# Optimization experiments

Hardware: AMD Instinct MI355X
Metric: run time of the kernel (lower is better)

The kernel has to match this reference:

```python
import jax, jax.numpy as jnp
import numpy as np

V = 32000   # vocab_size
T = 2048    # train_len (pos embed table size)
E = 1024    # embed_dim
H = 16      # num_heads
FF = 4096   # ff_dim
L = 4       # num_layers
B, C = 2, 1024
D = E // H  # head_dim = 64
EPS = 1e-5


def setup_inputs() -> dict:
    key = jax.random.key(0)
    ks = jax.random.split(key, 12)
    s = 0.02
    inp = {
        "x": jax.random.randint(ks[0], (B, C), 0, V),
        "embed": jax.random.normal(ks[1], (V, E), jnp.float32) * s,
        "pos_embed": jax.random.normal(ks[2], (T, E), jnp.float32) * s,
        "Wq": jax.random.normal(ks[3], (L, E, E), jnp.float32) * s,
        "Wk": jax.random.normal(ks[4], (L, E, E), jnp.float32) * s,
        "Wv": jax.random.normal(ks[5], (L, E, E), jnp.float32) * s,
        "Wo": jax.random.normal(ks[6], (L, E, E), jnp.float32) * s,
        "ln1_w": jnp.ones((L, E), jnp.float32),
        "ln1_b": jnp.zeros((L, E), jnp.float32),
        "ln2_w": jnp.ones((L, E), jnp.float32),
        "ln2_b": jnp.zeros((L, E), jnp.float32),
        "W1": jax.random.normal(ks[7], (L, E, FF), jnp.float32) * s,
        "b1": jnp.zeros((L, FF), jnp.float32),
        "W2": jax.random.normal(ks[8], (L, FF, E), jnp.float32) * s,
        "b2": jnp.zeros((L, E), jnp.float32),
        "lnf_w": jnp.ones((E,), jnp.float32),
        "lnf_b": jnp.zeros((E,), jnp.float32),
        "Wout": jax.random.normal(ks[9], (E, V), jnp.float32) * s,
        "bout": jnp.zeros((V,), jnp.float32),
    }
    return inp


def _layernorm(h, w, b):
    mu = jnp.mean(h, axis=-1, keepdims=True)
    var = jnp.var(h, axis=-1, keepdims=True)
    return (h - mu) * jax.lax.rsqrt(var + EPS) * w + b


def reference(x, embed, pos_embed, Wq, Wk, Wv, Wo, ln1_w, ln1_b, ln2_w, ln2_b,
              W1, b1, W2, b2, lnf_w, lnf_b, Wout, bout):
    Bx, Cx = x.shape
    positions = jnp.clip(jnp.arange(Cx), 0, T - 1)  # 'clamp' extrapolation
    h = embed[x] + pos_embed[positions]             # [B,C,E]
    # causal mask: -inf above the diagonal
    mask = jnp.where(jnp.tril(jnp.ones((Cx, Cx), bool)), 0.0, -jnp.inf).astype(h.dtype)
    scale = 1.0 / np.sqrt(D)
    for i in range(L):
        hn = _layernorm(h, ln1_w[i], ln1_b[i])
        Q = (hn @ Wq[i]).reshape(Bx, Cx, H, D).transpose(0, 2, 1, 3)  # [B,H,C,D]
        K = (hn @ Wk[i]).reshape(Bx, Cx, H, D).transpose(0, 2, 1, 3)
        Vv = (hn @ Wv[i]).reshape(Bx, Cx, H, D).transpose(0, 2, 1, 3)
        scores = jnp.einsum('bhqd,bhkd->bhqk', Q, K) * scale + mask
        weights = jax.nn.softmax(scores, axis=-1)
        attn = jnp.einsum('bhqk,bhkd->bhqd', weights, Vv)
        attn = attn.transpose(0, 2, 1, 3).reshape(Bx, Cx, E) @ Wo[i]
        h = h + attn
        hn2 = _layernorm(h, ln2_w[i], ln2_b[i])
        h = h + jax.nn.gelu(hn2 @ W1[i] + b1[i], approximate=False) @ W2[i] + b2[i]
    return _layernorm(h, lnf_w, lnf_b) @ Wout + bout  # [B,C,V]
```

## Files before the change

### kernel.cpp

```cpp
#include <hip/hip_runtime.h>
#include <hip/hip_bf16.h>
#include <math.h>

constexpr int V  = 32000;
constexpr int E  = 1024;
constexpr int H  = 16;
constexpr int FF = 4096;
constexpr int L  = 4;
constexpr int B  = 2;
constexpr int C  = 1024;
constexpr int D  = 64;
constexpr int N  = B * C;
constexpr int E3 = 3 * E;
constexpr float EPS = 1e-5f;

typedef __hip_bfloat16 bf16;
typedef __bf16 bf16x8 __attribute__((ext_vector_type(8)));
typedef __bf16 bf16x4 __attribute__((ext_vector_type(4)));
typedef float  f32x4  __attribute__((ext_vector_type(4)));

#define AS1 __attribute__((address_space(1)))
#define AS3 __attribute__((address_space(3)))

__device__ inline bf16x8 lds_load8(const bf16* p) {
    bf16x4 lo = *(const bf16x4*)p;
    bf16x4 hi = *(const bf16x4*)(p + 4);
    bf16x8 r;
    r[0]=lo[0]; r[1]=lo[1]; r[2]=lo[2]; r[3]=lo[3];
    r[4]=hi[0]; r[5]=hi[1]; r[6]=hi[2]; r[7]=hi[3];
    return r;
}
__device__ inline void lds_store8(bf16* p, bf16x8 v) {
    bf16x4 lo, hi;
    lo[0]=v[0]; lo[1]=v[1]; lo[2]=v[2]; lo[3]=v[3];
    hi[0]=v[4]; hi[1]=v[5]; hi[2]=v[6]; hi[3]=v[7];
    *(bf16x4*)p = lo; *(bf16x4*)(p + 4) = hi;
}

__device__ inline bf16x8 lds_frag(const bf16* sbase, int row, int chunk) {
    return *(const bf16x8*)(sbase + (row >> 3) * 512 + (row & 7) * 64 +
                            ((chunk ^ (row & 7)) << 3));
}

__global__ void embed_kernel(const int* __restrict__ x,
                             const float* __restrict__ embed,
                             const float* __restrict__ pos,
                             float* __restrict__ h) {
    int token = blockIdx.x;
    int c = token % C;
    int id = x[token];
    const float* erow = embed + (size_t)id * E;
    const float* prow = pos   + (size_t)c  * E;
    float* hrow = h + (size_t)token * E;
    for (int e = threadIdx.x; e < E; e += blockDim.x)
        hrow[e] = erow[e] + prow[e];
}

__global__ void layernorm_kernel(const float* __restrict__ in,
                                 const float* __restrict__ w,
                                 const float* __restrict__ b,
                                 bf16* __restrict__ out) {
    __shared__ float red[256];
    int token = blockIdx.x;
    int tid = threadIdx.x;
    float4 xv = ((const float4*)(in + (size_t)token * E))[tid];

    red[tid] = xv.x + xv.y + xv.z + xv.w;
    __syncthreads();
    for (int st = 128; st > 0; st >>= 1) {
        if (tid < st) red[tid] += red[tid + st];
        __syncthreads();
    }
    float mu = red[0] * (1.0f / E);
    __syncthreads();

    float d0 = xv.x - mu, d1 = xv.y - mu, d2 = xv.z - mu, d3 = xv.w - mu;
    red[tid] = d0 * d0 + d1 * d1 + d2 * d2 + d3 * d3;
    __syncthreads();
    for (int st = 128; st > 0; st >>= 1) {
        if (tid < st) red[tid] += red[tid + st];
        __syncthreads();
    }
    float var = red[0] * (1.0f / E);
    float inv = rsqrtf(var + EPS);

    float4 wv = ((const float4*)w)[tid];
    float4 bv = ((const float4*)b)[tid];
    float y0 = d0 * inv * wv.x + bv.x;
    float y1 = d1 * inv * wv.y + bv.y;
    float y2 = d2 * inv * wv.z + bv.z;
    float y3 = d3 * inv * wv.w + bv.w;
    ushort4 o;
    { bf16 t0 = __float2bfloat16(y0); o.x = *(ushort*)&t0; }
    { bf16 t1 = __float2bfloat16(y1); o.y = *(ushort*)&t1; }
    { bf16 t2 = __float2bfloat16(y2); o.z = *(ushort*)&t2; }
    { bf16 t3 = __float2bfloat16(y3); o.w = *(ushort*)&t3; }
    ((ushort4*)(out + (size_t)token * E))[tid] = o;
}

__global__ void transpose_bf16(const float* __restrict__ in,
                               bf16* __restrict__ out, int K, int Nn) {
    __shared__ float tile[32][33];
    int n0 = blockIdx.x * 32, k0 = blockIdx.y * 32;
    int tx = threadIdx.x & 31, ty = threadIdx.x >> 5;
    #pragma unroll
    for (int i = 0; i < 32; i += 8)
        tile[ty + i][tx] = in[(size_t)(k0 + ty + i) * Nn + n0 + tx];
    __syncthreads();
    #pragma unroll
    for (int i = 0; i < 32; i += 8)
        out[(size_t)(n0 + ty + i) * K + k0 + tx] = __float2bfloat16(tile[tx][ty + i]);
}

__global__ void transpose_v(const bf16* __restrict__ qkv,
                            bf16* __restrict__ vt) {
    __shared__ ushort tile[32][34];
    int c0 = blockIdx.x * 32;
    int d0 = (blockIdx.y & 1) * 32;
    int bh = blockIdx.y >> 1;
    int bb = bh >> 4, hh = bh & 15;
    int tx = threadIdx.x & 31, ty = threadIdx.x >> 5;
    const ushort* src = (const ushort*)qkv;
    ushort* dst = (ushort*)vt;
    #pragma unroll
    for (int i = 0; i < 32; i += 8)
        tile[ty + i][tx] = src[(size_t)(bb * C + c0 + ty + i) * E3 + 2 * E + hh * D + d0 + tx];
    __syncthreads();
    #pragma unroll
    for (int i = 0; i < 32; i += 8)
        dst[((size_t)bh * D + d0 + ty + i) * C + c0 + tx] = tile[tx][ty + i];
}

__launch_bounds__(256, 2)
__global__ void gemm_bf16_128(const bf16* __restrict__ A,
                              const bf16* __restrict__ Bt,
                              const float* __restrict__ bias,
                              const float* __restrict__ res,
                              float* __restrict__ outF,
                              bf16*  __restrict__ outB,
                              int M, int Nc, int K, int gelu_flag) {
    __shared__ __align__(16) bf16 sA[2][128 * 64];
    __shared__ __align__(16) bf16 sB[2][128 * 64];

    int tid  = threadIdx.x;
    int lane = tid & 63;
    int wid  = tid >> 6;
    int wr   = wid >> 1;
    int wc   = wid & 1;
    int l16  = lane & 15;
    int lhi  = lane >> 4;

    int nwg = gridDim.x * gridDim.y;
    int id  = blockIdx.y * gridDim.x + blockIdx.x;
    int cpx = nwg >> 3;
    int swz = (id & 7) * cpx + (id >> 3);
    int bx  = swz / gridDim.y;
    int by  = swz % gridDim.y;

    size_t brow = (size_t)by * 128;
    size_t bcol = (size_t)bx * 128;

    f32x4 acc[4][4] = {};

    auto stage = [&](int buf, int t) {
        size_t k0 = (size_t)t * 64;
        #pragma unroll
        for (int s = 0; s < 4; ++s) {
            int slot = s * 256 + tid;
            int row  = slot >> 3;
            int ch   = (slot & 7) ^ (row & 7);
            int ldso = (s * 256 + wid * 64) * 8;
            const bf16* ga = A + (brow + row) * K + k0 + ch * 8;
            __builtin_amdgcn_global_load_lds(
                (const AS1 void*)ga, (AS3 void*)(&sA[buf][0] + ldso), 16, 0, 0);
        }
        #pragma unroll
        for (int s = 0; s < 4; ++s) {
            int slot = s * 256 + tid;
            int row  = slot >> 3;
            int ch   = (slot & 7) ^ (row & 7);
            int ldso = (s * 256 + wid * 64) * 8;
            const bf16* gb = Bt + (bcol + row) * K + k0 + ch * 8;
            __builtin_amdgcn_global_load_lds(
                (const AS1 void*)gb, (AS3 void*)(&sB[buf][0] + ldso), 16, 0, 0);
        }
    };

    int NT = K / 64;
    stage(0, 0);

    for (int t = 0; t < NT; ++t) {
        if (t + 1 < NT) {
            stage((t + 1) & 1, t + 1);
            asm volatile("s_waitcnt vmcnt(8)" ::: "memory");
        } else {
            asm volatile("s_waitcnt vmcnt(0)" ::: "memory");
        }
        __builtin_amdgcn_sched_barrier(0);
        __builtin_amdgcn_s_barrier();

        const bf16* As_ = &sA[t & 1][0];
        const bf16* Bs_ = &sB[t & 1][0];
        bf16x8 ra[4][2], rb[4][2];
        #pragma unroll
        for (int m = 0; m < 4; ++m)
            #pragma unroll
            for (int kh = 0; kh < 2; ++kh)
                ra[m][kh] = lds_frag(As_, wr * 64 + m * 16 + l16, kh * 4 + lhi);
        #pragma unroll
        for (int n = 0; n < 4; ++n)
            #pragma unroll
            for (int kh = 0; kh < 2; ++kh)
                rb[n][kh] = lds_frag(Bs_, wc * 64 + n * 16 + l16, kh * 4 + lhi);

        __builtin_amdgcn_s_setprio(1);
        #pragma unroll
        for (int m = 0; m < 4; ++m)
            #pragma unroll
            for (int n = 0; n < 4; ++n)
                #pragma unroll
                for (int kh = 0; kh < 2; ++kh)
                    acc[m][n] = __builtin_amdgcn_mfma_f32_16x16x32_bf16(
                        ra[m][kh], rb[n][kh], acc[m][n], 0, 0, 0);
        __builtin_amdgcn_s_setprio(0);
        __builtin_amdgcn_s_barrier();
    }

    int crow = lhi * 4;
    #pragma unroll
    for (int m = 0; m < 4; ++m) {
        #pragma unroll
        for (int n = 0; n < 4; ++n) {
            #pragma unroll
            for (int r = 0; r < 4; ++r) {
                size_t row = brow + wr * 64 + m * 16 + crow + r;
                size_t col = bcol + wc * 64 + n * 16 + l16;
                float val = acc[m][n][r];
                if (bias) val += bias[col];
                if (gelu_flag) val = 0.5f * val * (1.0f + erff(val * 0.70710678118f));
                if (res) val += res[row * Nc + col];
                if (outF) outF[row * Nc + col] = val;
                if (outB) outB[row * Nc + col] = __float2bfloat16(val);
            }
        }
    }
}

__launch_bounds__(256, 3)
__global__ void gemm_bf16_64(const bf16* __restrict__ A,
                             const bf16* __restrict__ Bt,
                             const float* __restrict__ bias,
                             const float* __restrict__ res,
                             float* __restrict__ outF,
                             bf16*  __restrict__ outB,
                             int M, int Nc, int K, int gelu_flag) {
    __shared__ __align__(16) bf16 sA[2][64 * 64];
    __shared__ __align__(16) bf16 sB[2][128 * 64];

    int tid  = threadIdx.x;
    int lane = tid & 63;
    int wid  = tid >> 6;
    int l16  = lane & 15;
    int lhi  = lane >> 4;

    int nwg = gridDim.x * gridDim.y;
    int id  = blockIdx.y * gridDim.x + blockIdx.x;
    int cpx = nwg >> 3;
    int swz = (id & 7) * cpx + (id >> 3);
    int bx  = swz / gridDim.y;
    int by  = swz % gridDim.y;

    size_t brow = (size_t)by * 64;
    size_t bcol = (size_t)bx * 128;

    f32x4 acc[4][2] = {};

    auto stage = [&](int buf, int t) {
        size_t k0 = (size_t)t * 64;
        #pragma unroll
        for (int s = 0; s < 2; ++s) {
            int slot = s * 256 + tid;
            int row  = slot >> 3;
            int ch   = (slot & 7) ^ (row & 7);
            int ldso = (s * 256 + wid * 64) * 8;
            const bf16* ga = A + (brow + row) * K + k0 + ch * 8;
            __builtin_amdgcn_global_load_lds(
                (const AS1 void*)ga, (AS3 void*)(&sA[buf][0] + ldso), 16, 0, 0);
        }
        #pragma unroll
        for (int s = 0; s < 4; ++s) {
            int slot = s * 256 + tid;
            int row  = slot >> 3;
            int ch   = (slot & 7) ^ (row & 7);
            int ldso = (s * 256 + wid * 64) * 8;
            const bf16* gb = Bt + (bcol + row) * K + k0 + ch * 8;
            __builtin_amdgcn_global_load_lds(
                (const AS1 void*)gb, (AS3 void*)(&sB[buf][0] + ldso), 16, 0, 0);
        }
    };

    int NT = K / 64;
    stage(0, 0);

    for (int t = 0; t < NT; ++t) {
        if (t + 1 < NT) {
            stage((t + 1) & 1, t + 1);
            asm volatile("s_waitcnt vmcnt(6)" ::: "memory");
        } else {
            asm volatile("s_waitcnt vmcnt(0)" ::: "memory");
        }
        __builtin_amdgcn_sched_barrier(0);
        __builtin_amdgcn_s_barrier();

        const bf16* As_ = &sA[t & 1][0];
        const bf16* Bs_ = &sB[t & 1][0];
        bf16x8 ra[4][2], rb[2][2];
        #pragma unroll
        for (int m = 0; m < 4; ++m)
            #pragma unroll
            for (int kh = 0; kh < 2; ++kh)
                ra[m][kh] = lds_frag(As_, m * 16 + l16, kh * 4 + lhi);
        #pragma unroll
        for (int n = 0; n < 2; ++n)
            #pragma unroll
            for (int kh = 0; kh < 2; ++kh)
                rb[n][kh] = lds_frag(Bs_, wid * 32 + n * 16 + l16, kh * 4 + lhi);

        __builtin_amdgcn_s_setprio(1);
        #pragma unroll
        for (int m = 0; m < 4; ++m)
            #pragma unroll
            for (int n = 0; n < 2; ++n)
                #pragma unroll
                for (int kh = 0; kh < 2; ++kh)
                    acc[m][n] = __builtin_amdgcn_mfma_f32_16x16x32_bf16(
                        ra[m][kh], rb[n][kh], acc[m][n], 0, 0, 0);
        __builtin_amdgcn_s_setprio(0);
        __builtin_amdgcn_s_barrier();
    }

    int crow = lhi * 4;
    #pragma unroll
    for (int m = 0; m < 4; ++m) {
        #pragma unroll
        for (int n = 0; n < 2; ++n) {
            #pragma unroll
            for (int r = 0; r < 4; ++r) {
                size_t row = brow + m * 16 + crow + r;
                size_t col = bcol + wid * 32 + n * 16 + l16;
                float val = acc[m][n][r];
                if (bias) val += bias[col];
                if (gelu_flag) val = 0.5f * val * (1.0f + erff(val * 0.70710678118f));
                if (res) val += res[row * Nc + col];
                if (outF) outF[row * Nc + col] = val;
                if (outB) outB[row * Nc + col] = __float2bfloat16(val);
            }
        }
    }
}

constexpr int QBLK = 64;
constexpr int KVB  = 64;
constexpr int PSTR = 72;

__launch_bounds__(256)
__global__ void flash_attn(const bf16* __restrict__ qkv,
                           const bf16* __restrict__ vt,
                           bf16* __restrict__ O) {
    __shared__ bf16 sK[KVB][PSTR];
    __shared__ bf16 sV[D][PSTR];
    __shared__ bf16 sP[4][16][PSTR];

    int qt = blockIdx.x;
    int bh = blockIdx.y;
    int bb = bh >> 4, hh = bh & 15;
    int qbase = qt * QBLK;
    int tid = threadIdx.x, lane = tid & 63, w = tid >> 6;
    int l16 = lane & 15, lhi = lane >> 4;

    int qrow = qbase + w * 16 + l16;
    const bf16* qp = qkv + (size_t)(bb * C + qrow) * E3 + hh * D + lhi * 8;
    bf16x8 qf0 = *(const bf16x8*)qp;
    bf16x8 qf1 = *(const bf16x8*)(qp + 32);

    f32x4 oa[4] = {};
    float m_run[4] = {-INFINITY, -INFINITY, -INFINITY, -INFINITY};
    float l_run[4] = {0.f, 0.f, 0.f, 0.f};

    for (int t = 0; t <= qt; ++t) {
        int k0 = t * KVB;
        #pragma unroll
        for (int it = 0; it < 2; ++it) {
            int s = it * 256 + tid;
            int row = s >> 3, c8 = s & 7;
            bf16x8 kv = *(const bf16x8*)(qkv + (size_t)(bb * C + k0 + row) * E3 + E + hh * D + c8 * 8);
            lds_store8(&sK[row][c8 * 8], kv);
            bf16x8 vv = *(const bf16x8*)(vt + ((size_t)bh * D + row) * C + k0 + c8 * 8);
            lds_store8(&sV[row][c8 * 8], vv);
        }
        __syncthreads();

        f32x4 sc[4] = {};
        #pragma unroll
        for (int n = 0; n < 4; ++n) {
            bf16x8 kf0 = lds_load8(&sK[n * 16 + l16][lhi * 8]);
            sc[n] = __builtin_amdgcn_mfma_f32_16x16x32_bf16(qf0, kf0, sc[n], 0, 0, 0);
            bf16x8 kf1 = lds_load8(&sK[n * 16 + l16][32 + lhi * 8]);
            sc[n] = __builtin_amdgcn_mfma_f32_16x16x32_bf16(qf1, kf1, sc[n], 0, 0, 0);
        }

        int qg = qbase + w * 16 + lhi * 4;
        #pragma unroll
        for (int n = 0; n < 4; ++n) {
            int kg = k0 + n * 16 + l16;
            #pragma unroll
            for (int r = 0; r < 4; ++r) {
                float vvv = sc[n][r] * 0.125f;
                if (t == qt && kg > qg + r) vvv = -1e30f;
                sc[n][r] = vvv;
            }
        }

        float pm[4];
        #pragma unroll
        for (int r = 0; r < 4; ++r)
            pm[r] = fmaxf(fmaxf(sc[0][r], sc[1][r]), fmaxf(sc[2][r], sc[3][r]));
        #pragma unroll
        for (int xm = 1; xm <= 8; xm <<= 1)
            #pragma unroll
            for (int r = 0; r < 4; ++r)
                pm[r] = fmaxf(pm[r], __shfl_xor(pm[r], xm));

        float corr[4];
        #pragma unroll
        for (int r = 0; r < 4; ++r) {
            float mn = fmaxf(m_run[r], pm[r]);
            corr[r] = __expf(m_run[r] - mn);
            m_run[r] = mn;
        }
        f32x4 p[4];
        #pragma unroll
        for (int n = 0; n < 4; ++n)
            #pragma unroll
            for (int r = 0; r < 4; ++r)
                p[n][r] = __expf(sc[n][r] - m_run[r]);

        float rsum[4];
        #pragma unroll
        for (int r = 0; r < 4; ++r)
            rsum[r] = p[0][r] + p[1][r] + p[2][r] + p[3][r];
        #pragma unroll
        for (int xm = 1; xm <= 8; xm <<= 1)
            #pragma unroll
            for (int r = 0; r < 4; ++r)
                rsum[r] += __shfl_xor(rsum[r], xm);
        #pragma unroll
        for (int r = 0; r < 4; ++r)
            l_run[r] = l_run[r] * corr[r] + rsum[r];
        #pragma unroll
        for (int nd = 0; nd < 4; ++nd)
            #pragma unroll
            for (int r = 0; r < 4; ++r)
                oa[nd][r] *= corr[r];

        #pragma unroll
        for (int n = 0; n < 4; ++n)
            #pragma unroll
            for (int r = 0; r < 4; ++r)
                sP[w][lhi * 4 + r][n * 16 + l16] = __float2bfloat16(p[n][r]);
        bf16x8 pa0 = lds_load8(&sP[w][l16][lhi * 8]);
        bf16x8 pa1 = lds_load8(&sP[w][l16][32 + lhi * 8]);

        #pragma unroll
        for (int nd = 0; nd < 4; ++nd) {
            bf16x8 vf0 = lds_load8(&sV[nd * 16 + l16][lhi * 8]);
            oa[nd] = __builtin_amdgcn_mfma_f32_16x16x32_bf16(pa0, vf0, oa[nd], 0, 0, 0);
            bf16x8 vf1 = lds_load8(&sV[nd * 16 + l16][32 + lhi * 8]);
            oa[nd] = __builtin_amdgcn_mfma_f32_16x16x32_bf16(pa1, vf1, oa[nd], 0, 0, 0);
        }
        __syncthreads();
    }

    #pragma unroll
    for (int r = 0; r < 4; ++r) {
        float inv = 1.0f / l_run[r];
        int qg = qbase + w * 16 + lhi * 4 + r;
        bf16* orow = O + (size_t)(bb * C + qg) * E + hh * D;
        #pragma unroll
        for (int nd = 0; nd < 4; ++nd)
            orow[nd * 16 + l16] = __float2bfloat16(oa[nd][r] * inv);
    }
}

extern "C" void kernel_launch(void* const* d_in, const int* in_sizes, int n_in,
                              void* d_out, int out_size, void* d_ws, size_t ws_size,
                              hipStream_t stream) {
    const int*   x     = (const int*)  d_in[0];
    const float* embed = (const float*)d_in[1];
    const float* pos   = (const float*)d_in[2];
    const float* Wq    = (const float*)d_in[3];
    const float* Wk    = (const float*)d_in[4];
    const float* Wv    = (const float*)d_in[5];
    const float* Wo    = (const float*)d_in[6];
    const float* ln1w  = (const float*)d_in[7];
    const float* ln1b  = (const float*)d_in[8];
    const float* ln2w  = (const float*)d_in[9];
    const float* ln2b  = (const float*)d_in[10];
    const float* W1    = (const float*)d_in[11];
    const float* b1    = (const float*)d_in[12];
    const float* W2    = (const float*)d_in[13];
    const float* b2    = (const float*)d_in[14];
    const float* lnfw  = (const float*)d_in[15];
    const float* lnfb  = (const float*)d_in[16];
    const float* Wout  = (const float*)d_in[17];
    const float* bout  = (const float*)d_in[18];
    float* out = (float*)d_out;

    char* p = (char*)d_ws;
    auto alloc = [&](size_t bytes) {
        char* r = p;
        p += (bytes + 255) & ~(size_t)255;
        return r;
    };
    float* h    = (float*)alloc((size_t)N * E  * 4);
    bf16*  qkvb = (bf16*) alloc((size_t)N * E3 * 2);
    bf16*  hn   = (bf16*) alloc((size_t)N * E  * 2);
    bf16*  attn = (bf16*) alloc((size_t)N * E  * 2);
    bf16*  ff   = (bf16*) alloc((size_t)N * FF * 2);
    bf16*  vt   = (bf16*) alloc((size_t)B * H * D * C * 2);
    bf16*  qkvt = (bf16*) alloc((size_t)L * E3 * E * 2);
    bf16*  wot  = (bf16*) alloc((size_t)L * E  * E * 2);
    bf16*  w1t  = (bf16*) alloc((size_t)L * FF * E * 2);
    bf16*  w2t  = (bf16*) alloc((size_t)L * E  * FF * 2);
    bf16*  wvt  = (bf16*) alloc((size_t)V * E  * 2);

    for (int i = 0; i < L; ++i) {
        transpose_bf16<<<dim3(E / 32, E / 32), 256, 0, stream>>>(
            Wq + (size_t)i * E * E, qkvt + ((size_t)i * E3 + 0 * E) * E, E, E);
        transpose_bf16<<<dim3(E / 32, E / 32), 256, 0, stream>>>(
            Wk + (size_t)i * E * E, qkvt + ((size_t)i * E3 + 1 * E) * E, E, E);
        transpose_bf16<<<dim3(E / 32, E / 32), 256, 0, stream>>>(
            Wv + (size_t)i * E * E, qkvt + ((size_t)i * E3 + 2 * E) * E, E, E);
        transpose_bf16<<<dim3(E / 32, E / 32), 256, 0, stream>>>(
            Wo + (size_t)i * E * E, wot + (size_t)i * E * E, E, E);
        transpose_bf16<<<dim3(FF / 32, E / 32), 256, 0, stream>>>(
            W1 + (size_t)i * E * FF, w1t + (size_t)i * FF * E, E, FF);
        transpose_bf16<<<dim3(E / 32, FF / 32), 256, 0, stream>>>(
            W2 + (size_t)i * FF * E, w2t + (size_t)i * E * FF, FF, E);
    }
    transpose_bf16<<<dim3(V / 32, E / 32), 256, 0, stream>>>(Wout, wvt, E, V);

    embed_kernel<<<N, 256, 0, stream>>>(x, embed, pos, h);

    dim3 gQKV(E3 / 128, N / 128);
    dim3 gF  (FF / 128, N / 128);
    dim3 gV  (V  / 128, N / 128);
    dim3 gO  (E  / 128, N / 64);

    for (int i = 0; i < L; ++i) {
        layernorm_kernel<<<N, 256, 0, stream>>>(h, ln1w + i * E, ln1b + i * E, hn);

        gemm_bf16_128<<<gQKV, 256, 0, stream>>>(hn, qkvt + (size_t)i * E3 * E,
                                                nullptr, nullptr, nullptr, qkvb,
                                                N, E3, E, 0);

        transpose_v<<<dim3(C / 32, 2 * B * H), 256, 0, stream>>>(qkvb, vt);

        flash_attn<<<dim3(C / QBLK, B * H), 256, 0, stream>>>(qkvb, vt, attn);

        gemm_bf16_64<<<gO, 256, 0, stream>>>(attn, wot + (size_t)i * E * E,
                                             nullptr, h, h, nullptr,
                                             N, E, E, 0);

        layernorm_kernel<<<N, 256, 0, stream>>>(h, ln2w + i * E, ln2b + i * E, hn);

        gemm_bf16_128<<<gF, 256, 0, stream>>>(hn, w1t + (size_t)i * FF * E,
                                              b1 + (size_t)i * FF, nullptr,
                                              nullptr, ff,
                                              N, FF, E, 1);
        gemm_bf16_64<<<gO, 256, 0, stream>>>(ff, w2t + (size_t)i * E * FF,
                                             b2 + (size_t)i * E, h, h, nullptr,
                                             N, E, FF, 0);
    }

    layernorm_kernel<<<N, 256, 0, stream>>>(h, lnfw, lnfb, hn);
    gemm_bf16_128<<<gV, 256, 0, stream>>>(hn, wvt, bout, nullptr, out, nullptr,
                                          N, V, E, 0);
}
```

Measured before the change: 1.382 ms.

## Deepen GEMM prefetch with 4-stage K=32 ring and add 256x256 vocab GEMM

All bf16 GEMMs now use a K-step of 32 with a four-buffer LDS ring. Two stages are prefetched ahead via global_load_lds, and the trailing per-iteration barrier is dropped. The LDS swizzle is reworked to match the 32-wide rows. A new 512-thread 256x256-tile kernel handles the large vocabulary projection to raise data reuse per block. The cost is more LDS per block: the 256 kernel's roughly 128KB likely limits it to one block per CU despite launch bounds of 2. The K=32 steps also mean more barriers per unit of work.

```diff
diff --git a/kernel.cpp b/kernel.cpp
--- a/kernel.cpp
+++ b/kernel.cpp
@@ -33,13 +33,13 @@
 __device__ inline void lds_store8(bf16* p, bf16x8 v) {
     bf16x4 lo, hi;
     lo[0]=v[0]; lo[1]=v[1]; lo[2]=v[2]; lo[3]=v[3];
+    hi[0]=v[4]; hi[1]=v[5]; hi[2]=v[6]; hi[7-3]=v[7]; hi[2]=v[6];
     hi[0]=v[4]; hi[1]=v[5]; hi[2]=v[6]; hi[3]=v[7];
     *(bf16x4*)p = lo; *(bf16x4*)(p + 4) = hi;
 }
 
-__device__ inline bf16x8 lds_frag(const bf16* sbase, int row, int chunk) {
-    return *(const bf16x8*)(sbase + (row >> 3) * 512 + (row & 7) * 64 +
-                            ((chunk ^ (row & 7)) << 3));
+__device__ inline bf16x8 lds_frag32(const bf16* sbase, int row, int c) {
+    return *(const bf16x8*)(sbase + row * 32 + ((c ^ ((row >> 1) & 3)) << 3));
 }
 
 __global__ void embed_kernel(const int* __restrict__ x,
@@ -131,6 +131,118 @@
         dst[((size_t)bh * D + d0 + ty + i) * C + c0 + tx] = tile[tx][ty + i];
 }
 
+
+__launch_bounds__(512, 2)
+__global__ void gemm_bf16_256(const bf16* __restrict__ A,
+                              const bf16* __restrict__ Bt,
+                              const float* __restrict__ bias,
+                              const float* __restrict__ res,
+                              float* __restrict__ outF,
+                              bf16*  __restrict__ outB,
+                              int M, int Nc, int K, int gelu_flag) {
+    __shared__ __align__(16) bf16 sA[4][256 * 32];
+    __shared__ __align__(16) bf16 sB[4][256 * 32];
+
+    int tid  = threadIdx.x;
+    int lane = tid & 63;
+    int wid  = tid >> 6;
+    int wm   = wid >> 2;
+    int wn   = wid & 3;
+    int l16  = lane & 15;
+    int lhi  = lane >> 4;
+
+    int nwg = gridDim.x * gridDim.y;
+    int id  = blockIdx.y * gridDim.x + blockIdx.x;
+    int cpx = nwg >> 3;
+    int swz = (id & 7) * cpx + (id >> 3);
+    int bx  = swz / gridDim.y;
+    int by  = swz % gridDim.y;
+
+    size_t brow = (size_t)by * 256;
+    size_t bcol = (size_t)bx * 256;
+
+    f32x4 acc[8][4] = {};
+
+    auto stage = [&](int buf, int t) {
+        size_t k0 = (size_t)t * 32;
+        #pragma unroll
+        for (int j = 0; j < 2; ++j) {
+            int s = j * 512 + tid;
+            int row = s >> 2;
+            int ch  = (s & 3) ^ ((row >> 1) & 3);
+            int ldso = (j * 512 + wid * 64) * 8;
+            const bf16* ga = A + (brow + row) * K + k0 + ch * 8;
+            __builtin_amdgcn_global_load_lds(
+                (const AS1 void*)ga, (AS3 void*)(&sA[buf][0] + ldso), 16, 0, 0);
+        }
+        #pragma unroll
+        for (int j = 0; j < 2; ++j) {
+            int s = j * 512 + tid;
+            int row = s >> 2;
+            int ch  = (s & 3) ^ ((row >> 1) & 3);
+            int ldso = (j * 512 + wid * 64) * 8;
+            const bf16* gb = Bt + (bcol + row) * K + k0 + ch * 8;
+            __builtin_amdgcn_global_load_lds(
+                (const AS1 void*)gb, (AS3 void*)(&sB[buf][0] + ldso), 16, 0, 0);
+        }
+    };
+
+    int NT = K / 32;
+    stage(0, 0);
+    stage(1, 1);
+
+    for (int t = 0; t < NT; ++t) {
+        if (t + 2 < NT) {
+            stage((t + 2) & 3, t + 2);
+            asm volatile("s_waitcnt vmcnt(8)" ::: "memory");
+        } else if (t + 1 < NT) {
+            asm volatile("s_waitcnt vmcnt(4)" ::: "memory");
+        } else {
+            asm volatile("s_waitcnt vmcnt(0)" ::: "memory");
+        }
+        __builtin_amdgcn_sched_barrier(0);
+        __builtin_amdgcn_s_barrier();
+
+        const bf16* As_ = &sA[t & 3][0];
+        const bf16* Bs_ = &sB[t & 3][0];
+        bf16x8 ra[8], rb[4];
+        #pragma unroll
+        for (int m = 0; m < 8; ++m)
+            ra[m] = lds_frag32(As_, wm * 128 + m * 16 + l16, lhi);
+        #pragma unroll
+        for (int n = 0; n < 4; ++n)
+            rb[n] = lds_frag32(Bs_, wn * 64 + n * 16 + l16, lhi);
+
+        __builtin_amdgcn_s_setprio(1);
+        #pragma unroll
+        for (int m = 0; m < 8; ++m)
+            #pragma unroll
+            for (int n = 0; n < 4; ++n)
+                acc[m][n] = __builtin_amdgcn_mfma_f32_16x16x32_bf16(
+                    ra[m], rb[n], acc[m][n], 0, 0, 0);
+        __builtin_amdgcn_s_setprio(0);
+    }
+
+    int crow = lhi * 4;
+    #pragma unroll
+    for (int m = 0; m < 8; ++m) {
+        #pragma unroll
+        for (int n = 0; n < 4; ++n) {
+            #pragma unroll
+            for (int r = 0; r < 4; ++r) {
+                size_t row = brow + wm * 128 + m * 16 + crow + r;
+                size_t col = bcol + wn * 64 + n * 16 + l16;
+                float val = acc[m][n][r];
+                if (bias) val += bias[col];
+                if (gelu_flag) val = 0.5f * val * (1.0f + erff(val * 0.70710678118f));
+                if (res) val += res[row * Nc + col];
+                if (outF) outF[row * Nc + col] = val;
+                if (outB) outB[row * Nc + col] = __float2bfloat16(val);
+            }
+        }
+    }
+}
+
 __launch_bounds__(256, 2)
 __global__ void gemm_bf16_128(const bf16* __restrict__ A,
                               const bf16* __restrict__ Bt,
@@ -139,8 +251,8 @@
                               float* __restrict__ outF,
                               bf16*  __restrict__ outB,
                               int M, int Nc, int K, int gelu_flag) {
-    __shared__ __align__(16) bf16 sA[2][128 * 64];
-    __shared__ __align__(16) bf16 sB[2][128 * 64];
+    __shared__ __align__(16) bf16 sA[4][128 * 32];
+    __shared__ __align__(16) bf16 sB[4][128 * 32];
 
     int tid  = threadIdx.x;
     int lane = tid & 63;
@@ -163,67 +275,63 @@
     f32x4 acc[4][4] = {};
 
     auto stage = [&](int buf, int t) {
-        size_t k0 = (size_t)t * 64;
-        #pragma unroll
-        for (int s = 0; s < 4; ++s) {
-            int slot = s * 256 + tid;
-            int row  = slot >> 3;
-            int ch   = (slot & 7) ^ (row & 7);
-            int ldso = (s * 256 + wid * 64) * 8;
+        size_t k0 = (size_t)t * 32;
+        #pragma unroll
+        for (int j = 0; j < 2; ++j) {
+            int s = j * 256 + tid;
+            int row = s >> 2;
+            int ch  = (s & 3) ^ ((row >> 1) & 3);
+            int ldso = (j * 256 + wid * 64) * 8;
             const bf16* ga = A + (brow + row) * K + k0 + ch * 8;
             __builtin_amdgcn_global_load_lds(
                 (const AS1 void*)ga, (AS3 void*)(&sA[buf][0] + ldso), 16, 0, 0);
         }
         #pragma unroll
-        for (int s = 0; s < 4; ++s) {
-            int slot = s * 256 + tid;
-            int row  = slot >> 3;
-            int ch   = (slot & 7) ^ (row & 7);
-            int ldso = (s * 256 + wid * 64) * 8;
+        for (int j = 0; j < 2; ++j) {
+            int s = j * 256 + tid;
+            int row = s >> 2;
+            int ch  = (s & 3) ^ ((row >> 1) & 3);
+            int ldso = (j * 256 + wid * 64) * 8;
             const bf16* gb = Bt + (bcol + row) * K + k0 + ch * 8;
             __builtin_amdgcn_global_load_lds(
                 (const AS1 void*)gb, (AS3 void*)(&sB[buf][0] + ldso), 16, 0, 0);
         }
     };
 
-    int NT = K / 64;
+    int NT = K / 32;
     stage(0, 0);
+    stage(1, 1);
 
     for (int t = 0; t < NT; ++t) {
-        if (t + 1 < NT) {
-            stage((t + 1) & 1, t + 1);
+        if (t + 2 < NT) {
+            stage((t + 2) & 3, t + 2);
             asm volatile("s_waitcnt vmcnt(8)" ::: "memory");
+        } else if (t + 1 < NT) {
+            asm volatile("s_waitcnt vmcnt(4)" ::: "memory");
         } else {
             asm volatile("s_waitcnt vmcnt(0)" ::: "memory");
         }
         __builtin_amdgcn_sched_barrier(0);
         __builtin_amdgcn_s_barrier();
 
-        const bf16* As_ = &sA[t & 1][0];
-        const bf16* Bs_ = &sB[t & 1][0];
-        bf16x8 ra[4][2], rb[4][2];
+        const bf16* As_ = &sA[t & 3][0];
+        const bf16* Bs_ = &sB[t & 3][0];
+        bf16x8 ra[4], rb[4];
         #pragma unroll
         for (int m = 0; m < 4; ++m)
-            #pragma unroll
-            for (int kh = 0; kh < 2; ++kh)
-                ra[m][kh] = lds_frag(As_, wr * 64 + m * 16 + l16, kh * 4 + lhi);
+            ra[m] = lds_frag32(As_, wr * 64 + m * 16 + l16, lhi);
         #pragma unroll
         for (int n = 0; n < 4; ++n)
-            #pragma unroll
-            for (int kh = 0; kh < 2; ++kh)
-                rb[n][kh] = lds_frag(Bs_, wc * 64 + n * 16 + l16, kh * 4 + lhi);
+            rb[n] = lds_frag32(Bs_, wc * 64 + n * 16 + l16, lhi);
 
         __builtin_amdgcn_s_setprio(1);
         #pragma unroll
         for (int m = 0; m < 4; ++m)
             #pragma unroll
             for (int n = 0; n < 4; ++n)
-                #pragma unroll
-                for (int kh = 0; kh < 2; ++kh)
-                    acc[m][n] = __builtin_amdgcn_mfma_f32_16x16x32_bf16(
-                        ra[m][kh], rb[n][kh], acc[m][n], 0, 0, 0);
+                acc[m][n] = __builtin_amdgcn_mfma_f32_16x16x32_bf16(
+                    ra[m], rb[n], acc[m][n], 0, 0, 0);
         __builtin_amdgcn_s_setprio(0);
-        __builtin_amdgcn_s_barrier();
     }
 
     int crow = lhi * 4;
@@ -254,8 +362,8 @@
                              float* __restrict__ outF,
                              bf16*  __restrict__ outB,
                              int M, int Nc, int K, int gelu_flag) {
-    __shared__ __align__(16) bf16 sA[2][64 * 64];
-    __shared__ __align__(16) bf16 sB[2][128 * 64];
+    __shared__ __align__(16) bf16 sA[4][64 * 32];
+    __shared__ __align__(16) bf16 sB[4][128 * 32];
 
     int tid  = threadIdx.x;
     int lane = tid & 63;
@@ -276,67 +384,62 @@
     f32x4 acc[4][2] = {};
 
     auto stage = [&](int buf, int t) {
-        size_t k0 = (size_t)t * 64;
-        #pragma unroll
-        for (int s = 0; s < 2; ++s) {
-            int slot = s * 256 + tid;
-            int row  = slot >> 3;
-            int ch   = (slot & 7) ^ (row & 7);
-            int ldso = (s * 256 + wid * 64) * 8;
+        size_t k0 = (size_t)t * 32;
+        {
+            int s = tid;
+            int row = s >> 2;
+            int ch  = (s & 3) ^ ((row >> 1) & 3);
+            int ldso = (wid * 64) * 8;
             const bf16* ga = A + (brow + row) * K + k0 + ch * 8;
             __builtin_amdgcn_global_load_lds(
                 (const AS1 void*)ga, (AS3 void*)(&sA[buf][0] + ldso), 16, 0, 0);
         }
         #pragma unroll
-        for (int s = 0; s < 4; ++s) {
-            int slot = s * 256 + tid;
-            int row  = slot >> 3;
-            int ch   = (slot & 7) ^ (row & 7);
-            int ldso = (s * 256 + wid * 64) * 8;
+        for (int j = 0; j < 2; ++j) {
+            int s = j * 256 + tid;
+            int row = s >> 2;
+            int ch  = (s & 3) ^ ((row >> 1) & 3);
+            int ldso = (j * 256 + wid * 64) * 8;
             const bf16* gb = Bt + (bcol + row) * K + k0 + ch * 8;
             __builtin_amdgcn_global_load_lds(
                 (const AS1 void*)gb, (AS3 void*)(&sB[buf][0] + ldso), 16, 0, 0);
         }
     };
 
-    int NT = K / 64;
+    int NT = K / 32;
     stage(0, 0);
+    stage(1, 1);
 
     for (int t = 0; t < NT; ++t) {
-        if (t + 1 < NT) {
-            stage((t + 1) & 1, t + 1);
+        if (t + 2 < NT) {
+            stage((t + 2) & 3, t + 2);
             asm volatile("s_waitcnt vmcnt(6)" ::: "memory");
+        } else if (t + 1 < NT) {
+            asm volatile("s_waitcnt vmcnt(3)" ::: "memory");
         } else {
             asm volatile("s_waitcnt vmcnt(0)" ::: "memory");
         }
         __builtin_amdgcn_sched_barrier(0);
         __builtin_amdgcn_s_barrier();
 
-        const bf16* As_ = &sA[t & 1][0];
-        const bf16* Bs_ = &sB[t & 1][0];
-        bf16x8 ra[4][2], rb[2][2];
+        const bf16* As_ = &sA[t & 3][0];
+        const bf16* Bs_ = &sB[t & 3][0];
+        bf16x8 ra[4], rb[2];
         #pragma unroll
         for (int m = 0; m < 4; ++m)
-            #pragma unroll
-            for (int kh = 0; kh < 2; ++kh)
-                ra[m][kh] = lds_frag(As_, m * 16 + l16, kh * 4 + lhi);
+            ra[m] = lds_frag32(As_, m * 16 + l16, lhi);
         #pragma unroll
         for (int n = 0; n < 2; ++n)
-            #pragma unroll
-            for (int kh = 0; kh < 2; ++kh)
-                rb[n][kh] = lds_frag(Bs_, wid * 32 + n * 16 + l16, kh * 4 + lhi);
+            rb[n] = lds_frag32(Bs_, wid * 32 + n * 16 + l16, lhi);
 
         __builtin_amdgcn_s_setprio(1);
         #pragma unroll
         for (int m = 0; m < 4; ++m)
             #pragma unroll
             for (int n = 0; n < 2; ++n)
-                #pragma unroll
-                for (int kh = 0; kh < 2; ++kh)
-                    acc[m][n] = __builtin_amdgcn_mfma_f32_16x16x32_bf16(
-                        ra[m][kh], rb[n][kh], acc[m][n], 0, 0, 0);
+                acc[m][n] = __builtin_amdgcn_mfma_f32_16x16x32_bf16(
+                    ra[m], rb[n], acc[m][n], 0, 0, 0);
         __builtin_amdgcn_s_setprio(0);
-        __builtin_amdgcn_s_barrier();
     }
 
     int crow = lhi * 4;
@@ -554,7 +657,7 @@
 
     dim3 gQKV(E3 / 128, N / 128);
     dim3 gF  (FF / 128, N / 128);
-    dim3 gV  (V  / 128, N / 128);
+    dim3 gV  (V  / 256, N / 256);
     dim3 gO  (E  / 128, N / 64);
 
     for (int i = 0; i < L; ++i) {
@@ -584,6 +687,6 @@
     }
 
     layernorm_kernel<<<N, 256, 0, stream>>>(h, lnfw, lnfb, hn);
-    gemm_bf16_128<<<gV, 256, 0, stream>>>(hn, wvt, bout, nullptr, out, nullptr,
+    gemm_bf16_256<<<gV, 512, 0, stream>>>(hn, wvt, bout, nullptr, out, nullptr,
                                           N, V, E, 0);
 }
```

New measurement: 1.347 ms. 1.03x faster.
